# Kernel optimization log

Measured on AMD Instinct MI355X. Metric: run time of the kernel, lower is better.

Reference implementation:

```python
import jax, jax.numpy as jnp
import numpy as np

N_NODES = 25000
N_EDGES = 400000
D = 1024


def setup_inputs() -> dict:
    key = jax.random.key(0)
    ks = jax.random.split(key, 8)
    s = 1.0 / np.sqrt(D)
    return {
        "x": jax.random.normal(ks[0], (N_NODES, D), dtype=jnp.float32),
        "edge_src": jax.random.randint(ks[1], (N_EDGES,), 0, N_NODES, dtype=jnp.int32),
        "edge_dst": jax.random.randint(ks[2], (N_EDGES,), 0, N_NODES, dtype=jnp.int32),
        "W_self0": jax.random.normal(ks[3], (D, D), dtype=jnp.float32) * s,
        "W_neigh0": jax.random.normal(ks[4], (D, D), dtype=jnp.float32) * s,
        "b0": jnp.zeros((D,), dtype=jnp.float32),
        "W_self1": jax.random.normal(ks[5], (D, D), dtype=jnp.float32) * s,
        "W_neigh1": jax.random.normal(ks[6], (D, D), dtype=jnp.float32) * s,
        "b1": jnp.zeros((D,), dtype=jnp.float32),
    }


def _sage_layer(h, edge_src, edge_dst, deg_inv, W_self, W_neigh, b):
    # mean aggregation over in-neighbors: gather src feats, segment-sum by dst
    msg = h[edge_src]                                            # [E, d]
    agg = jax.ops.segment_sum(msg, edge_dst, num_segments=h.shape[0])  # [N, d]
    mean = agg * deg_inv[:, None]
    return h @ W_self + mean @ W_neigh + b


def reference(x, edge_src, edge_dst, W_self0, W_neigh0, b0, W_self1, W_neigh1, b1):
    N = x.shape[0]
    deg = jax.ops.segment_sum(jnp.ones_like(edge_dst, dtype=x.dtype), edge_dst, num_segments=N)
    deg_inv = 1.0 / jnp.maximum(deg, 1.0)  # isolated nodes -> 0 neighbor mean
    h = jax.nn.relu(_sage_layer(x, edge_src, edge_dst, deg_inv, W_self0, W_neigh0, b0))
    out = _sage_layer(h, edge_src, edge_dst, deg_inv, W_self1, W_neigh1, b1)
    return out
```

## Files before the change

kernel.cpp:

```cpp
#include <hip/hip_runtime.h>
#include <stdint.h>

#define NN 25000
#define NE 400000
#define DD 1024

typedef __attribute__((ext_vector_type(8))) short short8;
typedef __attribute__((ext_vector_type(4))) float f32x4;

__device__ __forceinline__ unsigned short f2bf(float f) {
  union { float f; uint32_t u; } v; v.f = f;
  uint32_t r = v.u + 0x7fffu + ((v.u >> 16) & 1u);
  return (unsigned short)(r >> 16);
}
__device__ __forceinline__ float bf2f(unsigned short h) {
  union { uint32_t u; float f; } v; v.u = ((uint32_t)h) << 16;
  return v.f;
}

__device__ __forceinline__ void gld_lds16(const void* g, void* l) {
  __builtin_amdgcn_global_load_lds(
      (const __attribute__((address_space(1))) void*)g,
      (__attribute__((address_space(3))) void*)l, 16, 0, 0);
}

__global__ __launch_bounds__(256) void k_cast_bf16(const float* __restrict__ in,
                                                   unsigned short* __restrict__ out,
                                                   int n8) {
  int i = blockIdx.x * blockDim.x + threadIdx.x;
  int stride = gridDim.x * blockDim.x;
  for (; i < n8; i += stride) {
    const float4* p = (const float4*)(in + (size_t)i * 8);
    float4 a = p[0], b = p[1];
    ushort4 r0, r1;
    r0.x = f2bf(a.x); r0.y = f2bf(a.y); r0.z = f2bf(a.z); r0.w = f2bf(a.w);
    r1.x = f2bf(b.x); r1.y = f2bf(b.y); r1.z = f2bf(b.z); r1.w = f2bf(b.w);
    ushort4* q = (ushort4*)(out + (size_t)i * 8);
    q[0] = r0; q[1] = r1;
  }
}

__global__ __launch_bounds__(256) void k_transcast(const float* __restrict__ W,
                                                   unsigned short* __restrict__ WT,
                                                   int kofs) {
  __shared__ unsigned short tile[64][66];
  int t = threadIdx.x;
  int k0 = blockIdx.x * 64, n0 = blockIdx.y * 64;
#pragma unroll
  for (int p = 0; p < 16; ++p) {
    int idx = p * 256 + t;
    int lr = idx >> 6, lc = idx & 63;
    tile[lr][lc] = f2bf(W[(size_t)(k0 + lr) * 1024 + n0 + lc]);
  }
  __syncthreads();
#pragma unroll
  for (int p = 0; p < 16; ++p) {
    int idx = p * 256 + t;
    int lr = idx >> 6, lc = idx & 63;
    WT[(size_t)(n0 + lr) * 2048 + kofs + k0 + lc] = tile[lc][lr];
  }
}

__global__ __launch_bounds__(256) void k_deg(const int* __restrict__ dst,
                                             int* __restrict__ deg, int E) {
  int i = blockIdx.x * blockDim.x + threadIdx.x;
  if (i < E) atomicAdd(&deg[dst[i]], 1);
}

__global__ __launch_bounds__(256) void k_scan1(const int* __restrict__ deg,
                                               int* __restrict__ rowptr,
                                               int* __restrict__ bsum, int N) {
  __shared__ int ws[4];
  int t = threadIdx.x, lane = t & 63, w = t >> 6;
  int i = blockIdx.x * 256 + t;
  int v = (i < N) ? deg[i] : 0;
  int x = v;
#pragma unroll
  for (int off = 1; off < 64; off <<= 1) {
    int y = __shfl_up(x, off);
    if (lane >= off) x += y;
  }
  if (lane == 63) ws[w] = x;
  __syncthreads();
  int wbase = 0;
#pragma unroll
  for (int j = 0; j < 3; ++j)
    if (w > j) wbase += ws[j];
  if (i < N) rowptr[i] = wbase + x - v;
  if (t == 255) bsum[blockIdx.x] = wbase + x;
}

__global__ __launch_bounds__(128) void k_scan2(const int* __restrict__ bsum,
                                               int* __restrict__ boff,
                                               int* __restrict__ rowptr_end, int nb) {
  __shared__ int ws[2];
  int t = threadIdx.x, lane = t & 63, w = t >> 6;
  int v = (t < nb) ? bsum[t] : 0;
  int x = v;
#pragma unroll
  for (int off = 1; off < 64; off <<= 1) {
    int y = __shfl_up(x, off);
    if (lane >= off) x += y;
  }
  if (lane == 63) ws[w] = x;
  __syncthreads();
  int wbase = (w == 1) ? ws[0] : 0;
  if (t < nb) boff[t] = wbase + x - v;
  if (t == 127) *rowptr_end = wbase + x;
}

__global__ __launch_bounds__(256) void k_scan3(const int* __restrict__ deg,
                                               const int* __restrict__ boff,
                                               int* __restrict__ rowptr,
                                               int* __restrict__ cursor,
                                               float* __restrict__ dinv, int N) {
  int i = blockIdx.x * 256 + threadIdx.x;
  if (i < N) {
    int r = rowptr[i] + boff[blockIdx.x];
    rowptr[i] = r;
    cursor[i] = r;
    dinv[i] = 1.0f / fmaxf((float)deg[i], 1.0f);
  }
}

__global__ __launch_bounds__(256) void k_fill(const int* __restrict__ src,
                                              const int* __restrict__ dst,
                                              int* __restrict__ cursor,
                                              int* __restrict__ srcs, int E) {
  int i = blockIdx.x * blockDim.x + threadIdx.x;
  if (i < E) {
    int p = atomicAdd(&cursor[dst[i]], 1);
    srcs[p] = src[i];
  }
}

__global__ __launch_bounds__(256) void k_agg(const unsigned short* __restrict__ h,
                                             const int* __restrict__ rowptr,
                                             const int* __restrict__ srcs,
                                             const float* __restrict__ deg_inv,
                                             unsigned short* __restrict__ mean, int N) {
  int node = blockIdx.x * 2 + (threadIdx.x >> 7);
  if (node >= N) return;
  int t = threadIdx.x & 127;
  int c = t * 8;
  int beg = rowptr[node], end = rowptr[node + 1];
  float a[8];
#pragma unroll
  for (int j = 0; j < 8; ++j) a[j] = 0.f;
  int e = beg;
  for (; e + 1 < end; e += 2) {
    int s0 = srcs[e], s1 = srcs[e + 1];
    short8 v0 = *(const short8*)(h + (size_t)s0 * DD + c);
    short8 v1 = *(const short8*)(h + (size_t)s1 * DD + c);
#pragma unroll
    for (int j = 0; j < 8; ++j)
      a[j] += bf2f((unsigned short)v0[j]) + bf2f((unsigned short)v1[j]);
  }
  if (e < end) {
    int s0 = srcs[e];
    short8 v0 = *(const short8*)(h + (size_t)s0 * DD + c);
#pragma unroll
    for (int j = 0; j < 8; ++j) a[j] += bf2f((unsigned short)v0[j]);
  }
  float di = deg_inv[node];
  short8 r;
#pragma unroll
  for (int j = 0; j < 8; ++j) r[j] = (short)f2bf(a[j] * di);
  *(short8*)(mean + (size_t)node * DD + c) = r;
}

template <bool RELU, bool OUT_BF16>
__global__ __launch_bounds__(512, 2) void k_gemm(const unsigned short* __restrict__ A1,
                                                 const unsigned short* __restrict__ A2,
                                                 const unsigned short* __restrict__ WT,
                                                 const float* __restrict__ bias,
                                                 void* __restrict__ Cout, int M) {
  __shared__ __align__(16) char ldsc[131072];
  const int t = threadIdx.x;
  const int lane = t & 63, wave = t >> 6;
  const int wm = wave >> 2, wn = wave & 3;
  const int fr = lane & 15, fq = lane >> 4;

  const int cpx = gridDim.x >> 3;
  const int g = (blockIdx.x & 7) * cpx + (blockIdx.x >> 3);
  const int bm = g >> 2, bn = g & 3;

  int sb = lane * 16;
  sb ^= ((sb >> 9) & 1) << 5;
  const int s_r = sb >> 6;
  const int s_k = (sb & 63) >> 1;

  int rd = fr * 64 + fq * 16;
  rd ^= ((rd >> 9) & 1) << 5;

  f32x4 acc[8][4];
#pragma unroll
  for (int m = 0; m < 8; ++m)
#pragma unroll
    for (int n = 0; n < 4; ++n) acc[m][n] = (f32x4){0.f, 0.f, 0.f, 0.f};

  auto stage_half = [&](int t1, int hi, int bufb) {
    const bool isA = hi < 2;
    const int half = hi & 1;
    const unsigned short* src;
    int stride, kb, row0;
    if (isA) {
      src = (t1 < 16) ? A1 : A2;
      stride = 1024;
      kb = (t1 & 15) * 64;
      row0 = bm * 256 + half * 128;
    } else {
      src = WT;
      stride = 2048;
      kb = t1 * 64;
      row0 = bn * 256 + half * 128;
    }
    char* lbase = ldsc + bufb + hi * 16384 + wave * 1024;
#pragma unroll
    for (int j = 0; j < 2; ++j) {
      int sub = j * 8 + wave;
      int msub = sub >> 1, ksub = sub & 1;
      int row = row0 + msub * 16 + s_r;
      if (isA && row > M - 1) row = M - 1;
      gld_lds16(src + (size_t)row * stride + kb + ksub * 32 + s_k, lbase + j * 8192);
    }
  };

#define PHASE(QM, QN, STAGE)                                                          \
  {                                                                                   \
    short8 av[4][2], bv[2][2];                                                        \
    _Pragma("unroll") for (int im = 0; im < 4; ++im)                                  \
        _Pragma("unroll") for (int ks = 0; ks < 2; ++ks)                              \
            av[im][ks] = *(const short8*)(pa + (((QM) * 4 + im) * 2 + ks) * 1024);    \
    _Pragma("unroll") for (int in = 0; in < 2; ++in)                                  \
        _Pragma("unroll") for (int ks = 0; ks < 2; ++ks)                              \
            bv[in][ks] = *(const short8*)(pb + (((QN) * 2 + in) * 2 + ks) * 1024);    \
    STAGE;                                                                            \
    __builtin_amdgcn_s_barrier();                                                     \
    __builtin_amdgcn_s_setprio(1);                                                    \
    _Pragma("unroll") for (int im = 0; im < 4; ++im)                                  \
        _Pragma("unroll") for (int in = 0; in < 2; ++in)                              \
            _Pragma("unroll") for (int ks = 0; ks < 2; ++ks)                          \
                acc[(QM) * 4 + im][(QN) * 2 + in] =                                   \
                    __builtin_amdgcn_mfma_f32_16x16x32_bf16(                          \
                        av[im][ks], bv[in][ks], acc[(QM) * 4 + im][(QN) * 2 + in],    \
                        0, 0, 0);                                                     \
    __builtin_amdgcn_s_setprio(0);                                                    \
  }

  stage_half(0, 0, 0);
  stage_half(0, 1, 0);
  stage_half(0, 2, 0);
  stage_half(0, 3, 0);
  asm volatile("s_waitcnt vmcnt(0)" ::: "memory");
  __builtin_amdgcn_s_barrier();

#pragma unroll 1
  for (int kt = 0; kt < 32; ++kt) {
    const int cbuf = (kt & 1) << 16;
    const int nbuf = cbuf ^ 65536;
    const bool pf = kt < 31;
    const char* pa = ldsc + cbuf + wm * 16384 + rd;
    const char* pb = ldsc + cbuf + 32768 + (wn >> 1) * 16384 + (wn & 1) * 8192 + rd;

    PHASE(0, 0, if (pf) { stage_half(kt + 1, 0, nbuf); stage_half(kt + 1, 1, nbuf); })
    __builtin_amdgcn_s_barrier();
    PHASE(0, 1, if (pf) stage_half(kt + 1, 2, nbuf);)
    __builtin_amdgcn_s_barrier();
    PHASE(1, 0, if (pf) stage_half(kt + 1, 3, nbuf);)
    __builtin_amdgcn_s_barrier();
    PHASE(1, 1, ;)
    asm volatile("s_waitcnt vmcnt(0)" ::: "memory");
    __builtin_amdgcn_s_barrier();
  }
#undef PHASE

#pragma unroll
  for (int mf = 0; mf < 8; ++mf) {
    int r0 = bm * 256 + wm * 128 + mf * 16 + fq * 4;
#pragma unroll
    for (int j = 0; j < 4; ++j) {
      int r = r0 + j;
      if (r >= M) continue;
#pragma unroll
      for (int nf = 0; nf < 4; ++nf) {
        int c = bn * 256 + wn * 64 + nf * 16 + fr;
        float v = acc[mf][nf][j] + bias[c];
        if (RELU) v = fmaxf(v, 0.f);
        if (OUT_BF16)
          ((unsigned short*)Cout)[(size_t)r * 1024 + c] = f2bf(v);
        else
          ((float*)Cout)[(size_t)r * 1024 + c] = v;
      }
    }
  }
}

extern "C" void kernel_launch(void* const* d_in, const int* in_sizes, int n_in,
                              void* d_out, int out_size, void* d_ws, size_t ws_size,
                              hipStream_t stream) {
  const float* x = (const float*)d_in[0];
  const int* esrc = (const int*)d_in[1];
  const int* edst = (const int*)d_in[2];
  const float* Ws0 = (const float*)d_in[3];
  const float* Wn0 = (const float*)d_in[4];
  const float* b0 = (const float*)d_in[5];
  const float* Ws1 = (const float*)d_in[6];
  const float* Wn1 = (const float*)d_in[7];
  const float* b1 = (const float*)d_in[8];
  float* out = (float*)d_out;

  char* ws = (char*)d_ws;
  size_t off = 0;
  auto alloc = [&](size_t bytes) -> void* {
    void* p = ws + off;
    off = (off + bytes + 255) & ~(size_t)255;
    return p;
  };
  unsigned short* x_bf = (unsigned short*)alloc((size_t)NN * DD * 2);
  unsigned short* h_bf = (unsigned short*)alloc((size_t)NN * DD * 2);
  unsigned short* mean_bf = (unsigned short*)alloc((size_t)NN * DD * 2);
  unsigned short* WT0 = (unsigned short*)alloc((size_t)DD * 2048 * 2);
  unsigned short* WT1 = (unsigned short*)alloc((size_t)DD * 2048 * 2);
  int* deg = (int*)alloc((size_t)NN * 4);
  int* rowptr = (int*)alloc((size_t)(NN + 1) * 4);
  int* cursor = (int*)alloc((size_t)NN * 4);
  float* dinv = (float*)alloc((size_t)NN * 4);
  int* srcs = (int*)alloc((size_t)NE * 4);
  int* bsum = (int*)alloc(128 * 4);
  int* boff = (int*)alloc(128 * 4);

  hipMemsetAsync(deg, 0, (size_t)NN * 4, stream);

  k_cast_bf16<<<2048, 256, 0, stream>>>(x, x_bf, NN * DD / 8);
  dim3 tg(16, 16);
  k_transcast<<<tg, 256, 0, stream>>>(Ws0, WT0, 0);
  k_transcast<<<tg, 256, 0, stream>>>(Wn0, WT0, 1024);
  k_transcast<<<tg, 256, 0, stream>>>(Ws1, WT1, 0);
  k_transcast<<<tg, 256, 0, stream>>>(Wn1, WT1, 1024);

  const int nsb = (NN + 255) / 256;
  k_deg<<<(NE + 255) / 256, 256, 0, stream>>>(edst, deg, NE);
  k_scan1<<<nsb, 256, 0, stream>>>(deg, rowptr, bsum, NN);
  k_scan2<<<1, 128, 0, stream>>>(bsum, boff, rowptr + NN, nsb);
  k_scan3<<<nsb, 256, 0, stream>>>(deg, boff, rowptr, cursor, dinv, NN);
  k_fill<<<(NE + 255) / 256, 256, 0, stream>>>(esrc, edst, cursor, srcs, NE);

  const int nbm = (NN + 255) / 256;
  dim3 gg(nbm * 4);

  k_agg<<<(NN + 1) / 2, 256, 0, stream>>>(x_bf, rowptr, srcs, dinv, mean_bf, NN);
  k_gemm<true, true><<<gg, 512, 0, stream>>>(x_bf, mean_bf, WT0, b0, (void*)h_bf, NN);

  k_agg<<<(NN + 1) / 2, 256, 0, stream>>>(h_bf, rowptr, srcs, dinv, mean_bf, NN);
  k_gemm<false, false><<<gg, 512, 0, stream>>>(h_bf, mean_bf, WT1, b1, (void*)out, NN);
}
```

Baseline: 749.3 us.

## Deepen GEMM pipeline to 4-stage K=32 ring with partial waits; unroll aggregation by 4

```diff
diff --git a/kernel.cpp b/kernel.cpp
--- a/kernel.cpp
+++ b/kernel.cpp
@@ -148,15 +148,18 @@
 #pragma unroll
   for (int j = 0; j < 8; ++j) a[j] = 0.f;
   int e = beg;
-  for (; e + 1 < end; e += 2) {
-    int s0 = srcs[e], s1 = srcs[e + 1];
+  for (; e + 3 < end; e += 4) {
+    int s0 = srcs[e], s1 = srcs[e + 1], s2 = srcs[e + 2], s3 = srcs[e + 3];
     short8 v0 = *(const short8*)(h + (size_t)s0 * DD + c);
     short8 v1 = *(const short8*)(h + (size_t)s1 * DD + c);
+    short8 v2 = *(const short8*)(h + (size_t)s2 * DD + c);
+    short8 v3 = *(const short8*)(h + (size_t)s3 * DD + c);
 #pragma unroll
     for (int j = 0; j < 8; ++j)
-      a[j] += bf2f((unsigned short)v0[j]) + bf2f((unsigned short)v1[j]);
-  }
-  if (e < end) {
+      a[j] += (bf2f((unsigned short)v0[j]) + bf2f((unsigned short)v1[j])) +
+              (bf2f((unsigned short)v2[j]) + bf2f((unsigned short)v3[j]));
+  }
+  for (; e < end; ++e) {
     int s0 = srcs[e];
     short8 v0 = *(const short8*)(h + (size_t)s0 * DD + c);
 #pragma unroll
@@ -199,79 +202,68 @@
 #pragma unroll
     for (int n = 0; n < 4; ++n) acc[m][n] = (f32x4){0.f, 0.f, 0.f, 0.f};
 
-  auto stage_half = [&](int t1, int hi, int bufb) {
-    const bool isA = hi < 2;
-    const int half = hi & 1;
+  auto stage_half = [&](int t1, int which) {
+    char* buf = ldsc + ((t1 & 3) << 15);
+    const int half = which & 1;
     const unsigned short* src;
     int stride, kb, row0;
-    if (isA) {
-      src = (t1 < 16) ? A1 : A2;
+    if (which < 2) {
+      src = (t1 < 32) ? A1 : A2;
       stride = 1024;
-      kb = (t1 & 15) * 64;
+      kb = (t1 & 31) * 32;
       row0 = bm * 256 + half * 128;
     } else {
       src = WT;
       stride = 2048;
-      kb = t1 * 64;
+      kb = t1 * 32;
       row0 = bn * 256 + half * 128;
     }
-    char* lbase = ldsc + bufb + hi * 16384 + wave * 1024;
-#pragma unroll
-    for (int j = 0; j < 2; ++j) {
-      int sub = j * 8 + wave;
-      int msub = sub >> 1, ksub = sub & 1;
-      int row = row0 + msub * 16 + s_r;
-      if (isA && row > M - 1) row = M - 1;
-      gld_lds16(src + (size_t)row * stride + kb + ksub * 32 + s_k, lbase + j * 8192);
-    }
+    int row = row0 + wave * 16 + s_r;
+    if (which < 2 && row > M - 1) row = M - 1;
+    char* dst = buf + (which >> 1) * 16384 + half * 8192 + wave * 1024;
+    gld_lds16(src + (size_t)row * stride + kb + s_k, dst);
   };
 
-#define PHASE(QM, QN, STAGE)                                                          \
-  {                                                                                   \
-    short8 av[4][2], bv[2][2];                                                        \
-    _Pragma("unroll") for (int im = 0; im < 4; ++im)                                  \
-        _Pragma("unroll") for (int ks = 0; ks < 2; ++ks)                              \
-            av[im][ks] = *(const short8*)(pa + (((QM) * 4 + im) * 2 + ks) * 1024);    \
-    _Pragma("unroll") for (int in = 0; in < 2; ++in)                                  \
-        _Pragma("unroll") for (int ks = 0; ks < 2; ++ks)                              \
-            bv[in][ks] = *(const short8*)(pb + (((QN) * 2 + in) * 2 + ks) * 1024);    \
-    STAGE;                                                                            \
-    __builtin_amdgcn_s_barrier();                                                     \
-    __builtin_amdgcn_s_setprio(1);                                                    \
-    _Pragma("unroll") for (int im = 0; im < 4; ++im)                                  \
-        _Pragma("unroll") for (int in = 0; in < 2; ++in)                              \
-            _Pragma("unroll") for (int ks = 0; ks < 2; ++ks)                          \
-                acc[(QM) * 4 + im][(QN) * 2 + in] =                                   \
-                    __builtin_amdgcn_mfma_f32_16x16x32_bf16(                          \
-                        av[im][ks], bv[in][ks], acc[(QM) * 4 + im][(QN) * 2 + in],    \
-                        0, 0, 0);                                                     \
-    __builtin_amdgcn_s_setprio(0);                                                    \
-  }
-
-  stage_half(0, 0, 0);
-  stage_half(0, 1, 0);
-  stage_half(0, 2, 0);
-  stage_half(0, 3, 0);
-  asm volatile("s_waitcnt vmcnt(0)" ::: "memory");
-  __builtin_amdgcn_s_barrier();
+#define PHASE(QM, STAGE)                                                           \
+  {                                                                                \
+    short8 av[4], bv[4];                                                           \
+    _Pragma("unroll") for (int im = 0; im < 4; ++im)                               \
+        av[im] = *(const short8*)(pa + ((QM) * 4 + im) * 1024);                    \
+    _Pragma("unroll") for (int nf = 0; nf < 4; ++nf)                               \
+        bv[nf] = *(const short8*)(pb + nf * 1024);                                 \
+    STAGE;                                                                         \
+    __builtin_amdgcn_s_barrier();                                                  \
+    __builtin_amdgcn_s_setprio(1);                                                 \
+    _Pragma("unroll") for (int im = 0; im < 4; ++im)                               \
+        _Pragma("unroll") for (int nf = 0; nf < 4; ++nf)                           \
+            acc[(QM) * 4 + im][nf] = __builtin_amdgcn_mfma_f32_16x16x32_bf16(      \
+                av[im], bv[nf], acc[(QM) * 4 + im][nf], 0, 0, 0);                  \
+    __builtin_amdgcn_s_setprio(0);                                                 \
+  }
+
+#pragma unroll
+  for (int pt = 0; pt < 3; ++pt) {
+    stage_half(pt, 0); stage_half(pt, 1); stage_half(pt, 2); stage_half(pt, 3);
+  }
 
 #pragma unroll 1
-  for (int kt = 0; kt < 32; ++kt) {
-    const int cbuf = (kt & 1) << 16;
-    const int nbuf = cbuf ^ 65536;
-    const bool pf = kt < 31;
-    const char* pa = ldsc + cbuf + wm * 16384 + rd;
-    const char* pb = ldsc + cbuf + 32768 + (wn >> 1) * 16384 + (wn & 1) * 8192 + rd;
-
-    PHASE(0, 0, if (pf) { stage_half(kt + 1, 0, nbuf); stage_half(kt + 1, 1, nbuf); })
+  for (int kt = 0; kt < 64; ++kt) {
+    if (kt < 62)
+      asm volatile("s_waitcnt vmcnt(8)" ::: "memory");
+    else if (kt == 62)
+      asm volatile("s_waitcnt vmcnt(4)" ::: "memory");
+    else
+      asm volatile("s_waitcnt vmcnt(0)" ::: "memory");
+    __builtin_amdgcn_sched_barrier(0);
     __builtin_amdgcn_s_barrier();
-    PHASE(0, 1, if (pf) stage_half(kt + 1, 2, nbuf);)
+
+    const char* pa = ldsc + ((kt & 3) << 15) + wm * 8192 + rd;
+    const char* pb = ldsc + ((kt & 3) << 15) + 16384 + wn * 4096 + rd;
+    const bool pf = kt < 61;
+
+    PHASE(0, if (pf) { stage_half(kt + 3, 0); stage_half(kt + 3, 1); })
     __builtin_amdgcn_s_barrier();
-    PHASE(1, 0, if (pf) stage_half(kt + 1, 3, nbuf);)
-    __builtin_amdgcn_s_barrier();
-    PHASE(1, 1, ;)
-    asm volatile("s_waitcnt vmcnt(0)" ::: "memory");
-    __builtin_amdgcn_s_barrier();
+    PHASE(1, if (pf) { stage_half(kt + 3, 2); stage_half(kt + 3, 3); })
   }
 #undef PHASE
 
```

Measured after the change: 740.2 us. About the same (-1.2%).
